# Optimization experiments

Measured on AMD Instinct MI355X. Metric: run time of the kernel, lower is better.

The kernel has to match this reference:

```python
import jax, jax.numpy as jnp
import numpy as np

SS = 25.0 / 255.0   # spatial_scale = 1 / (SEARCH_SIZE/25), SEARCH_SIZE = 255
OUT = 7             # ROIPOOL_OUTSIZE // 4, ROIPOOL_OUTSIZE = 28
SP = 4              # sample_per_part (mmdet DeformRoIPooling default)
TRANS_STD = 0.1


def _deform_roi_pool(x, rois, offset):
    # x: [B,C,H,W]; rois: [N,5] (batch_idx,x1,y1,x2,y2); offset: [N,2,OUT,OUT] (ch0=x, ch1=y)
    B, C, H, W = x.shape
    N = rois.shape[0]
    b = rois[:, 0].astype(jnp.int32)
    sw = jnp.round(rois[:, 1]) * SS - 0.5
    sh = jnp.round(rois[:, 2]) * SS - 0.5
    rw = jnp.maximum((jnp.round(rois[:, 3]) + 1.0) * SS - 0.5 - sw, 0.1)
    rh = jnp.maximum((jnp.round(rois[:, 4]) + 1.0) * SS - 0.5 - sh, 0.1)
    bw, bh = rw / OUT, rh / OUT
    p = jnp.arange(OUT, dtype=x.dtype)
    tx = offset[:, 0] * TRANS_STD  # [N,OUT,OUT] indexed [n,ph,pw]
    ty = offset[:, 1] * TRANS_STD
    wstart = p[None, None, :] * bw[:, None, None] + sw[:, None, None] + tx * rw[:, None, None]
    hstart = p[None, :, None] * bh[:, None, None] + sh[:, None, None] + ty * rh[:, None, None]
    s = jnp.arange(SP, dtype=x.dtype)
    # sample coords [N,OUT,OUT,SP(ih),SP(iw)]
    sx = wstart[..., None, None] + s[None, None, None, None, :] * (bw / SP)[:, None, None, None, None]
    sy = hstart[..., None, None] + s[None, None, None, :, None] * (bh / SP)[:, None, None, None, None]
    valid = (sx >= -0.5) & (sx <= W - 0.5) & (sy >= -0.5) & (sy <= H - 0.5)
    xc = jnp.clip(sx, 0.0, W - 1.0)
    yc = jnp.clip(sy, 0.0, H - 1.0)
    x0 = jnp.floor(xc)
    y0 = jnp.floor(yc)
    dx = xc - x0
    dy = yc - y0
    xi0 = x0.astype(jnp.int32)
    yi0 = y0.astype(jnp.int32)
    xi1 = jnp.ceil(xc).astype(jnp.int32)
    yi1 = jnp.ceil(yc).astype(jnp.int32)
    feat = jnp.transpose(x, (0, 2, 3, 1))  # [B,H,W,C]
    bb = b[:, None, None, None, None]

    def g(yi, xi):
        return feat[bb, yi, xi]  # [N,OUT,OUT,SP,SP,C]

    val = (((1 - dx) * (1 - dy))[..., None] * g(yi0, xi0)
           + (dx * (1 - dy))[..., None] * g(yi0, xi1)
           + ((1 - dx) * dy)[..., None] * g(yi1, xi0)
           + (dx * dy)[..., None] * g(yi1, xi1))
    val = jnp.where(valid[..., None], val, 0.0)
    cnt = valid.sum(axis=(3, 4)).astype(x.dtype)              # [N,OUT,OUT]
    pooled = val.sum(axis=(3, 4)) / jnp.maximum(cnt, 1.0)[..., None]
    return jnp.transpose(pooled, (0, 3, 1, 2))                # [N,C,OUT,OUT]


def _lin(h, w, b):
    return h @ w.T + b


def _forward(x, rois, off_w1, off_b1, off_w2, off_b2, off_w3, off_b3,
             fc1_w, fc1_b, fc2_w, fc2_b, box_w, box_b):
    N = rois.shape[0]
    zero_off = jnp.zeros((N, 2, OUT, OUT), x.dtype)
    # pass 1: no-trans pooling -> offset prediction
    p0 = _deform_roi_pool(x, rois, zero_off).reshape(N, -1)
    h = jax.nn.relu(_lin(p0, off_w1, off_b1))
    h = jax.nn.relu(_lin(h, off_w2, off_b2))
    off = _lin(h, off_w3, off_b3).reshape(N, 2, OUT, OUT)
    # pass 2: deformable pooling with predicted offsets
    p = _deform_roi_pool(x, rois, off).reshape(N, -1)
    h = jax.nn.relu(_lin(p, fc1_w, fc1_b))
    h = jax.nn.relu(_lin(h, fc2_w, fc2_b))
    return _lin(h, box_w, box_b)  # [N,4]


def setup_inputs():
    key = jax.random.key(0)
    ks = jax.random.split(key, 16)
    B, C, H, W, N = 8, 256, 25, 25, 256
    IN = C * OUT * OUT  # 12544
    DFC, FCC = 1024, 512
    x = jax.random.normal(ks[0], (B, C, H, W), jnp.float32)
    bidx = jax.random.randint(ks[1], (N,), 0, B).astype(jnp.float32)
    x1 = jax.random.uniform(ks[2], (N,), minval=0.0, maxval=180.0)
    y1 = jax.random.uniform(ks[3], (N,), minval=0.0, maxval=180.0)
    wd = jax.random.uniform(ks[4], (N,), minval=24.0, maxval=120.0)
    ht = jax.random.uniform(ks[5], (N,), minval=24.0, maxval=120.0)
    rois = jnp.stack([bidx, x1, y1, jnp.clip(x1 + wd, 0.0, 254.0),
                      jnp.clip(y1 + ht, 0.0, 254.0)], axis=1)

    def lin_p(k, o, i):
        return jax.random.normal(k, (o, i), jnp.float32) * (1.0 / np.sqrt(i))

    return dict(
        x=x, rois=rois,
        off_w1=lin_p(ks[6], DFC, IN), off_b1=jnp.zeros((DFC,), jnp.float32),
        off_w2=lin_p(ks[7], DFC, DFC), off_b2=jnp.zeros((DFC,), jnp.float32),
        off_w3=lin_p(ks[8], 2 * OUT * OUT, DFC) * 0.1,
        off_b3=jnp.zeros((2 * OUT * OUT,), jnp.float32),
        fc1_w=lin_p(ks[9], FCC, IN), fc1_b=jnp.zeros((FCC,), jnp.float32),
        fc2_w=lin_p(ks[10], FCC, FCC), fc2_b=jnp.zeros((FCC,), jnp.float32),
        box_w=lin_p(ks[11], 4, FCC) * 0.001, box_b=jnp.zeros((4,), jnp.float32),
    )


def reference(x, rois, off_w1, off_b1, off_w2, off_b2, off_w3, off_b3,
              fc1_w, fc1_b, fc2_w, fc2_b, box_w, box_b):
    return _forward(x, rois, off_w1, off_b1, off_w2, off_b2, off_w3, off_b3,
                    fc1_w, fc1_b, fc2_w, fc2_b, box_w, box_b)
```

## Files before the change

kernel.cpp:

```cpp
#include <hip/hip_runtime.h>
#include <hip/hip_bf16.h>


#define NROI 256
#define NB   8
#define INF  12544
#define DFC  1024
#define FCC  512

typedef __attribute__((ext_vector_type(8))) short short8;
typedef __attribute__((ext_vector_type(4))) float floatx4;

static __device__ __forceinline__ unsigned short f2bf(float f) {
    unsigned int u = __float_as_uint(f);
    unsigned int r = (u + 0x7fffu + ((u >> 16) & 1u)) >> 16;
    return (unsigned short)r;
}

static __device__ __forceinline__ void async_copy16(const void* g, void* l) {
    __builtin_amdgcn_global_load_lds(
        (const __attribute__((address_space(1))) unsigned int*)g,
        (__attribute__((address_space(3))) unsigned int*)l, 16, 0, 0);
}

__global__ __launch_bounds__(256) void transpose_kernel(
        const float* __restrict__ x, float* __restrict__ xT) {
    __shared__ float t[32][33];
    int b  = blockIdx.z;
    int cb = blockIdx.y * 32;
    int lb = blockIdx.x * 32;
    int tx = threadIdx.x & 31, ty = threadIdx.x >> 5;
#pragma unroll
    for (int r = 0; r < 4; ++r) {
        int c = cb + ty + r * 8, l = lb + tx;
        if (l < 625) t[ty + r * 8][tx] = x[(size_t)(b * 256 + c) * 625 + l];
    }
    __syncthreads();
#pragma unroll
    for (int r = 0; r < 4; ++r) {
        int l = lb + ty + r * 8, c = cb + tx;
        if (l < 625) xT[((size_t)b * 625 + l) * 256 + c] = t[tx][ty + r * 8];
    }
}

__global__ __launch_bounds__(256) void pool_kernel(
        const float* __restrict__ feat, const float* __restrict__ rois,
        const float* __restrict__ off, int has_off,
        unsigned short* __restrict__ P) {
    __shared__ float sGrid[49][16];
    __shared__ int   sBase[49];
    __shared__ unsigned short sOut[128 * 49];
    const float SSC = (float)(25.0 / 255.0);
    int q = blockIdx.x;
    int n = blockIdx.y;
    int tid = threadIdx.x;

    if (tid < 49) {
        int bin = tid;
        const float* r = rois + n * 5;
        int b = (int)r[0];
        float sw = rintf(r[1]) * SSC - 0.5f;
        float sh = rintf(r[2]) * SSC - 0.5f;
        float rw = fmaxf((rintf(r[3]) + 1.0f) * SSC - 0.5f - sw, 0.1f);
        float rh = fmaxf((rintf(r[4]) + 1.0f) * SSC - 0.5f - sh, 0.1f);
        float bw = rw / 7.0f, bh = rh / 7.0f;
        float bws = bw * 0.25f, bhs = bh * 0.25f;
        int ph = bin / 7, pw = bin - ph * 7;
        float tx = 0.f, ty = 0.f;
        if (has_off) {
            tx = off[n * 98 + bin] * 0.1f;
            ty = off[n * 98 + 49 + bin] * 0.1f;
        }
        float wstart = pw * bw + sw + tx * rw;
        float hstart = ph * bh + sh + ty * rh;
#pragma unroll
        for (int i = 0; i < 16; ++i) sGrid[bin][i] = 0.f;
        int gy0 = 0, gx0 = 0, cnt = 0;
#pragma unroll
        for (int s = 0; s < 16; ++s) {
            float fx = wstart + (s & 3) * bws;
            float fy = hstart + (s >> 2) * bhs;
            bool valid = (fx >= -0.5f) && (fx <= 24.5f) && (fy >= -0.5f) && (fy <= 24.5f);
            float xc = fminf(fmaxf(fx, 0.f), 24.f);
            float yc = fminf(fmaxf(fy, 0.f), 24.f);
            float x0f = floorf(xc), y0f = floorf(yc);
            float dx = xc - x0f, dy = yc - y0f;
            int x0 = (int)x0f, y0 = (int)y0f;
            int x1 = (int)ceilf(xc), y1 = (int)ceilf(yc);
            if (s == 0) { gy0 = y0; gx0 = x0; }
            float w00 = (1.f - dx) * (1.f - dy), w01 = dx * (1.f - dy);
            float w10 = (1.f - dx) * dy,         w11 = dx * dy;
            if (!valid) { w00 = w01 = w10 = w11 = 0.f; }
            cnt += valid ? 1 : 0;
            int ry0 = (y0 - gy0) * 4, ry1 = (y1 - gy0) * 4;
            sGrid[bin][ry0 + (x0 - gx0)] += w00;
            sGrid[bin][ry0 + (x1 - gx0)] += w01;
            sGrid[bin][ry1 + (x0 - gx0)] += w10;
            sGrid[bin][ry1 + (x1 - gx0)] += w11;
        }
        float inv = 1.0f / fmaxf((float)cnt, 1.0f);
#pragma unroll
        for (int i = 0; i < 16; ++i) sGrid[bin][i] *= inv;
        sBase[bin] = gy0 | (gx0 << 8) | (b << 16);
    }
    __syncthreads();

    int wv = tid >> 6, lane = tid & 63;
    int cbase = q * 128 + lane * 2;
    for (int bin = wv; bin < 49; bin += 4) {
        int base = sBase[bin];
        int gy0 = base & 255, gx0 = (base >> 8) & 255, b = base >> 16;
        const float4* wp = (const float4*)sGrid[bin];
        float4 w0 = wp[0], w1 = wp[1], w2 = wp[2], w3 = wp[3];
        float ww[16] = { w0.x, w0.y, w0.z, w0.w, w1.x, w1.y, w1.z, w1.w,
                         w2.x, w2.y, w2.z, w2.w, w3.x, w3.y, w3.z, w3.w };
        int rowOff[4], colOff[4];
#pragma unroll
        for (int r = 0; r < 4; ++r) {
            rowOff[r] = min(gy0 + r, 24) * 25;
            colOff[r] = min(gx0 + r, 24);
        }
        int b625 = b * 625;
        float ax = 0.f, ay = 0.f;
#pragma unroll
        for (int cell = 0; cell < 16; ++cell) {
            int pix = b625 + rowOff[cell >> 2] + colOff[cell & 3];
            float2 v = *(const float2*)(feat + (size_t)pix * 256 + cbase);
            ax += ww[cell] * v.x;
            ay += ww[cell] * v.y;
        }
        sOut[(lane * 2) * 49 + bin] = f2bf(ax);
        sOut[(lane * 2 + 1) * 49 + bin] = f2bf(ay);
    }
    __syncthreads();
    const uint2* so = (const uint2*)sOut;
    uint2* dp = (uint2*)(P + (size_t)n * INF + q * 128 * 49);
    for (int i = tid; i < 128 * 49 / 4; i += 256) dp[i] = so[i];
}

__global__ __launch_bounds__(256) void gemm_pipe(
        const unsigned short* __restrict__ A, const float* __restrict__ Bw,
        float* __restrict__ Cpart, int N, int K, int kSteps) {
    constexpr int BM = 256, BN = 32, D = 3;
    constexpr int FM = 4, FN = 2;
    __shared__ unsigned short As[D][BM * 32];
    __shared__ float          Bs[D][BN * 32];
    const int tid = threadIdx.x;
    const int lane = tid & 63;
    const int wave = tid >> 6;
    const int n0 = blockIdx.x * BN;
    const int k0 = blockIdx.z * kSteps * 32;
    const int quad = lane >> 4;
    const int l16 = lane & 15;

    floatx4 acc[FM][FN];
#pragma unroll
    for (int i = 0; i < FM; ++i)
#pragma unroll
        for (int j = 0; j < FN; ++j) acc[i][j] = (floatx4)0.f;

    const unsigned short* ag[4];
    int albase[4];
#pragma unroll
    for (int i = 0; i < 4; ++i) {
        int idx = tid + i * 256;
        int row = idx >> 2;
        int kg4 = (idx & 3) ^ ((row >> 1) & 3);
        ag[i] = A + (size_t)row * K + kg4 * 8;
        albase[i] = (i * 256 + wave * 64) * 16;
    }
    const int brow = tid >> 3;
    const int bkg = (tid & 7) ^ ((brow >> 1) & 7);
    const float* bg = Bw + (size_t)(n0 + brow) * K + bkg * 4;
    const int blbase = wave * 64 * 16;

    auto issue = [&](int slot, int kk) {
#pragma unroll
        for (int i = 0; i < 4; ++i)
            async_copy16(ag[i] + kk, (char*)&As[slot][0] + albase[i]);
        async_copy16(bg + kk, (char*)&Bs[slot][0] + blbase);
    };

#pragma unroll
    for (int p = 0; p < D - 1; ++p) {
        int pk = (p < kSteps) ? p : (kSteps - 1);
        issue(p, k0 + pk * 32);
    }

    int cur = 0;
    for (int ks = 0; ks < kSteps; ++ks) {
        asm volatile("s_waitcnt vmcnt(5)" ::: "memory");
        asm volatile("s_barrier" ::: "memory");
        int pfs = cur + D - 1; if (pfs >= D) pfs -= D;
        int pfk = ks + D - 1; if (pfk >= kSteps) pfk = kSteps - 1;
        issue(pfs, k0 + pfk * 32);
        short8 a[FM], bf[FN];
#pragma unroll
        for (int i = 0; i < FM; ++i) {
            int r = wave * 64 + i * 16 + l16;
            int sl = quad ^ ((r >> 1) & 3);
            a[i] = *(const short8*)(&As[cur][0] + r * 32 + sl * 8);
        }
#pragma unroll
        for (int j = 0; j < FN; ++j) {
            int r = j * 16 + l16;
            int sw8 = (r >> 1) & 7;
            int g0 = (quad * 2) ^ sw8;
            int g1 = (quad * 2 + 1) ^ sw8;
            float4 v0 = *(const float4*)(&Bs[cur][0] + r * 32 + g0 * 4);
            float4 v1 = *(const float4*)(&Bs[cur][0] + r * 32 + g1 * 4);
            bf[j][0] = (short)f2bf(v0.x); bf[j][1] = (short)f2bf(v0.y);
            bf[j][2] = (short)f2bf(v0.z); bf[j][3] = (short)f2bf(v0.w);
            bf[j][4] = (short)f2bf(v1.x); bf[j][5] = (short)f2bf(v1.y);
            bf[j][6] = (short)f2bf(v1.z); bf[j][7] = (short)f2bf(v1.w);
        }
#pragma unroll
        for (int i = 0; i < FM; ++i)
#pragma unroll
            for (int j = 0; j < FN; ++j)
                acc[i][j] = __builtin_amdgcn_mfma_f32_16x16x32_bf16(a[i], bf[j], acc[i][j], 0, 0, 0);
        cur = cur + 1; if (cur >= D) cur = 0;
    }
    float* Cp = Cpart + (size_t)blockIdx.z * BM * N;
#pragma unroll
    for (int i = 0; i < FM; ++i)
#pragma unroll
        for (int rr = 0; rr < 4; ++rr) {
            int row = wave * 64 + i * 16 + quad * 4 + rr;
            float* cr = Cp + (size_t)row * N + n0;
#pragma unroll
            for (int j = 0; j < FN; ++j)
                cr[j * 16 + l16] = acc[i][j][rr];
        }
}

__global__ __launch_bounds__(256) void reduce_bias(
        const float* __restrict__ part, int zc, int mn4,
        const float* __restrict__ bias, int nmask, int relu,
        unsigned short* __restrict__ obf, float* __restrict__ of) {
    int idx = blockIdx.x * 256 + threadIdx.x;
    if (idx >= mn4) return;
    int idx4 = idx * 4;
    const float* bp = bias + (idx4 & nmask);
    float4 acc = *(const float4*)bp;
    const float4* p = (const float4*)part + idx;
    for (int z = 0; z < zc; ++z) {
        float4 v = p[(size_t)z * mn4];
        acc.x += v.x; acc.y += v.y; acc.z += v.z; acc.w += v.w;
    }
    if (relu) {
        acc.x = fmaxf(acc.x, 0.f); acc.y = fmaxf(acc.y, 0.f);
        acc.z = fmaxf(acc.z, 0.f); acc.w = fmaxf(acc.w, 0.f);
    }
    if (obf) {
        ushort4 h;
        h.x = f2bf(acc.x); h.y = f2bf(acc.y); h.z = f2bf(acc.z); h.w = f2bf(acc.w);
        *(ushort4*)(obf + idx4) = h;
    }
    if (of) *(float4*)(of + idx4) = acc;
}

__global__ __launch_bounds__(256) void fc_small(
        const float* __restrict__ h2, const float* __restrict__ w3,
        const float* __restrict__ b3, float* __restrict__ out) {
    __shared__ float shl[2][1024];
    int n2 = blockIdx.x * 2;
    int tid = threadIdx.x;
    for (int i = tid; i < 2048; i += 256)
        shl[i >> 10][i & 1023] = fmaxf(h2[(size_t)n2 * 1024 + i], 0.f);
    __syncthreads();
    int h = tid >> 7, o = tid & 127;
    if (o < 98) {
        float acc = b3[o];
        const float* w = w3 + (size_t)o * 1024;
        const float* s = shl[h];
        for (int k = 0; k < 1024; k += 4) {
            float4 wv = *(const float4*)(w + k);
            acc += s[k] * wv.x + s[k + 1] * wv.y + s[k + 2] * wv.z + s[k + 3] * wv.w;
        }
        out[(n2 + h) * 98 + o] = acc;
    }
}

__global__ __launch_bounds__(64) void head_kernel(
        const float* __restrict__ h4, const float* __restrict__ bw,
        const float* __restrict__ bb, float* __restrict__ out) {
    int n = blockIdx.x, t = threadIdx.x;
    float a0 = 0, a1 = 0, a2 = 0, a3 = 0;
    for (int k = t; k < 512; k += 64) {
        float v = fmaxf(h4[(size_t)n * 512 + k], 0.f);
        a0 += v * bw[k]; a1 += v * bw[512 + k];
        a2 += v * bw[1024 + k]; a3 += v * bw[1536 + k];
    }
#pragma unroll
    for (int o = 32; o > 0; o >>= 1) {
        a0 += __shfl_down(a0, o); a1 += __shfl_down(a1, o);
        a2 += __shfl_down(a2, o); a3 += __shfl_down(a3, o);
    }
    if (t == 0) {
        out[n * 4 + 0] = a0 + bb[0]; out[n * 4 + 1] = a1 + bb[1];
        out[n * 4 + 2] = a2 + bb[2]; out[n * 4 + 3] = a3 + bb[3];
    }
}

extern "C" void kernel_launch(void* const* d_in, const int* in_sizes, int n_in,
                              void* d_out, int out_size, void* d_ws, size_t ws_size,
                              hipStream_t stream) {
    const float* x      = (const float*)d_in[0];
    const float* rois   = (const float*)d_in[1];
    const float* off_w1 = (const float*)d_in[2];
    const float* off_b1 = (const float*)d_in[3];
    const float* off_w2 = (const float*)d_in[4];
    const float* off_b2 = (const float*)d_in[5];
    const float* off_w3 = (const float*)d_in[6];
    const float* off_b3 = (const float*)d_in[7];
    const float* fc1_w  = (const float*)d_in[8];
    const float* fc1_b  = (const float*)d_in[9];
    const float* fc2_w  = (const float*)d_in[10];
    const float* fc2_b  = (const float*)d_in[11];
    const float* box_w  = (const float*)d_in[12];
    const float* box_b  = (const float*)d_in[13];
    float* out = (float*)d_out;

    char* ws = (char*)d_ws;
    size_t o = 0;
    auto carve = [&](size_t bytes) { char* p = ws + o; o += (bytes + 255) & ~(size_t)255; return p; };
    float*          xT   = (float*)carve((size_t)NB * 625 * 256 * 4);
    unsigned short* P    = (unsigned short*)carve((size_t)NROI * INF * 2);
    unsigned short* h1b  = (unsigned short*)carve((size_t)NROI * DFC * 2);
    float*          h2   = (float*)carve((size_t)NROI * DFC * 4);
    float*          offb = (float*)carve((size_t)NROI * 98 * 4);
    unsigned short* h3b  = (unsigned short*)carve((size_t)NROI * FCC * 2);
    float*          h4   = (float*)carve((size_t)NROI * FCC * 4);
    size_t fixed = o;
    const size_t SLAB = (size_t)NROI * DFC * 4;
    int zg1;
    if      (ws_size >= fixed + 28 * SLAB) zg1 = 28;
    else if (ws_size >= fixed + 14 * SLAB) zg1 = 14;
    else                                   zg1 = 7;
    float* part = (float*)carve((size_t)zg1 * SLAB);

    transpose_kernel<<<dim3(20, 8, 8), 256, 0, stream>>>(x, xT);
    pool_kernel<<<dim3(2, NROI), 256, 0, stream>>>(xT, rois, nullptr, 0, P);
    gemm_pipe<<<dim3(32, 1, zg1), 256, 0, stream>>>(P, off_w1, part, DFC, INF, 392 / zg1);
    reduce_bias<<<256, 256, 0, stream>>>(part, zg1, NROI * DFC / 4, off_b1, DFC - 1, 1, h1b, nullptr);
    gemm_pipe<<<dim3(32, 1, 8), 256, 0, stream>>>(h1b, off_w2, part, DFC, DFC, 4);
    reduce_bias<<<256, 256, 0, stream>>>(part, 8, NROI * DFC / 4, off_b2, DFC - 1, 0, nullptr, h2);
    fc_small<<<128, 256, 0, stream>>>(h2, off_w3, off_b3, offb);
    pool_kernel<<<dim3(2, NROI), 256, 0, stream>>>(xT, rois, offb, 1, P);
    gemm_pipe<<<dim3(16, 1, zg1), 256, 0, stream>>>(P, fc1_w, part, FCC, INF, 392 / zg1);
    reduce_bias<<<128, 256, 0, stream>>>(part, zg1, NROI * FCC / 4, fc1_b, FCC - 1, 1, h3b, nullptr);
    gemm_pipe<<<dim3(16, 1, 8), 256, 0, stream>>>(h3b, fc2_w, part, FCC, FCC, 2);
    reduce_bias<<<128, 256, 0, stream>>>(part, 8, NROI * FCC / 4, fc2_b, FCC - 1, 0, nullptr, h4);
    head_kernel<<<NROI, 64, 0, stream>>>(h4, box_w, box_b, out);
}
```

Baseline: 302.7 us.

## Fuse all stages into one persistent kernel with atomic grid barriers

```diff
diff --git a/kernel.cpp b/kernel.cpp
--- a/kernel.cpp
+++ b/kernel.cpp
@@ -23,36 +23,53 @@
         (__attribute__((address_space(3))) unsigned int*)l, 16, 0, 0);
 }
 
-__global__ __launch_bounds__(256) void transpose_kernel(
-        const float* __restrict__ x, float* __restrict__ xT) {
-    __shared__ float t[32][33];
-    int b  = blockIdx.z;
-    int cb = blockIdx.y * 32;
-    int lb = blockIdx.x * 32;
-    int tx = threadIdx.x & 31, ty = threadIdx.x >> 5;
-#pragma unroll
-    for (int r = 0; r < 4; ++r) {
-        int c = cb + ty + r * 8, l = lb + tx;
-        if (l < 625) t[ty + r * 8][tx] = x[(size_t)(b * 256 + c) * 625 + l];
-    }
-    __syncthreads();
-#pragma unroll
-    for (int r = 0; r < 4; ++r) {
-        int l = lb + ty + r * 8, c = cb + tx;
-        if (l < 625) xT[((size_t)b * 625 + l) * 256 + c] = t[tx][ty + r * 8];
-    }
-}
-
-__global__ __launch_bounds__(256) void pool_kernel(
+union SMem {
+    struct { float t[32][33]; } tr;
+    struct { float grid[49][16]; int base[49];
+             unsigned short out[128 * 49]; } pool;
+    struct { unsigned short As[3][256 * 32]; float Bs[3][32 * 32]; } gm;
+    struct { float h[1024]; } fc;
+};
+
+static __device__ __forceinline__ void gridbar(unsigned* ctr, int idx, unsigned nblk) {
+    __syncthreads();
+    if (threadIdx.x == 0) {
+        __hip_atomic_fetch_add(&ctr[idx], 1u, __ATOMIC_ACQ_REL, __HIP_MEMORY_SCOPE_AGENT);
+        while (__hip_atomic_load(&ctr[idx], __ATOMIC_ACQUIRE, __HIP_MEMORY_SCOPE_AGENT) < nblk)
+            __builtin_amdgcn_s_sleep(1);
+    }
+    __syncthreads();
+}
+
+static __device__ __forceinline__ void phase_transpose(
+        const float* __restrict__ x, float* __restrict__ xT, SMem& sm) {
+    int tid = threadIdx.x;
+    int tx = tid & 31, ty = tid >> 5;
+    for (int t = blockIdx.x; t < 1280; t += gridDim.x) {
+        int b = t / 160, rem = t - b * 160;
+        int cb = (rem / 20) * 32, lb = (rem % 20) * 32;
+#pragma unroll
+        for (int r = 0; r < 4; ++r) {
+            int c = cb + ty + r * 8, l = lb + tx;
+            if (l < 625) sm.tr.t[ty + r * 8][tx] = x[(size_t)(b * 256 + c) * 625 + l];
+        }
+        __syncthreads();
+#pragma unroll
+        for (int r = 0; r < 4; ++r) {
+            int l = lb + ty + r * 8, c = cb + tx;
+            if (l < 625) xT[((size_t)b * 625 + l) * 256 + c] = sm.tr.t[tx][ty + r * 8];
+        }
+        __syncthreads();
+    }
+}
+
+static __device__ __forceinline__ void phase_pool(
         const float* __restrict__ feat, const float* __restrict__ rois,
         const float* __restrict__ off, int has_off,
-        unsigned short* __restrict__ P) {
-    __shared__ float sGrid[49][16];
-    __shared__ int   sBase[49];
-    __shared__ unsigned short sOut[128 * 49];
+        unsigned short* __restrict__ P, SMem& sm) {
     const float SSC = (float)(25.0 / 255.0);
-    int q = blockIdx.x;
-    int n = blockIdx.y;
+    int q = blockIdx.x >> 8;
+    int n = blockIdx.x & 255;
     int tid = threadIdx.x;
 
     if (tid < 49) {
@@ -74,7 +91,7 @@
         float wstart = pw * bw + sw + tx * rw;
         float hstart = ph * bh + sh + ty * rh;
 #pragma unroll
-        for (int i = 0; i < 16; ++i) sGrid[bin][i] = 0.f;
+        for (int i = 0; i < 16; ++i) sm.pool.grid[bin][i] = 0.f;
         int gy0 = 0, gx0 = 0, cnt = 0;
 #pragma unroll
         for (int s = 0; s < 16; ++s) {
@@ -93,24 +110,24 @@
             if (!valid) { w00 = w01 = w10 = w11 = 0.f; }
             cnt += valid ? 1 : 0;
             int ry0 = (y0 - gy0) * 4, ry1 = (y1 - gy0) * 4;
-            sGrid[bin][ry0 + (x0 - gx0)] += w00;
-            sGrid[bin][ry0 + (x1 - gx0)] += w01;
-            sGrid[bin][ry1 + (x0 - gx0)] += w10;
-            sGrid[bin][ry1 + (x1 - gx0)] += w11;
+            sm.pool.grid[bin][ry0 + (x0 - gx0)] += w00;
+            sm.pool.grid[bin][ry0 + (x1 - gx0)] += w01;
+            sm.pool.grid[bin][ry1 + (x0 - gx0)] += w10;
+            sm.pool.grid[bin][ry1 + (x1 - gx0)] += w11;
         }
         float inv = 1.0f / fmaxf((float)cnt, 1.0f);
 #pragma unroll
-        for (int i = 0; i < 16; ++i) sGrid[bin][i] *= inv;
-        sBase[bin] = gy0 | (gx0 << 8) | (b << 16);
+        for (int i = 0; i < 16; ++i) sm.pool.grid[bin][i] *= inv;
+        sm.pool.base[bin] = gy0 | (gx0 << 8) | (b << 16);
     }
     __syncthreads();
 
     int wv = tid >> 6, lane = tid & 63;
     int cbase = q * 128 + lane * 2;
     for (int bin = wv; bin < 49; bin += 4) {
-        int base = sBase[bin];
+        int base = sm.pool.base[bin];
         int gy0 = base & 255, gx0 = (base >> 8) & 255, b = base >> 16;
-        const float4* wp = (const float4*)sGrid[bin];
+        const float4* wp = (const float4*)sm.pool.grid[bin];
         float4 w0 = wp[0], w1 = wp[1], w2 = wp[2], w3 = wp[3];
         float ww[16] = { w0.x, w0.y, w0.z, w0.w, w1.x, w1.y, w1.z, w1.w,
                          w2.x, w2.y, w2.z, w2.w, w3.x, w3.y, w3.z, w3.w };
@@ -129,35 +146,33 @@
             ax += ww[cell] * v.x;
             ay += ww[cell] * v.y;
         }
-        sOut[(lane * 2) * 49 + bin] = f2bf(ax);
-        sOut[(lane * 2 + 1) * 49 + bin] = f2bf(ay);
-    }
-    __syncthreads();
-    const uint2* so = (const uint2*)sOut;
+        sm.pool.out[(lane * 2) * 49 + bin] = f2bf(ax);
+        sm.pool.out[(lane * 2 + 1) * 49 + bin] = f2bf(ay);
+    }
+    __syncthreads();
+    const uint2* so = (const uint2*)sm.pool.out;
     uint2* dp = (uint2*)(P + (size_t)n * INF + q * 128 * 49);
     for (int i = tid; i < 128 * 49 / 4; i += 256) dp[i] = so[i];
 }
 
-__global__ __launch_bounds__(256) void gemm_pipe(
+static __device__ __forceinline__ void gemm_phase(
         const unsigned short* __restrict__ A, const float* __restrict__ Bw,
-        float* __restrict__ Cpart, int N, int K, int kSteps) {
-    constexpr int BM = 256, BN = 32, D = 3;
-    constexpr int FM = 4, FN = 2;
-    __shared__ unsigned short As[D][BM * 32];
-    __shared__ float          Bs[D][BN * 32];
+        float* __restrict__ Cpart, int N, int K, int nT, int zN, SMem& sm) {
+    const int blk = blockIdx.x;
+    if (blk >= nT * zN) return;
     const int tid = threadIdx.x;
-    const int lane = tid & 63;
-    const int wave = tid >> 6;
-    const int n0 = blockIdx.x * BN;
-    const int k0 = blockIdx.z * kSteps * 32;
-    const int quad = lane >> 4;
-    const int l16 = lane & 15;
-
-    floatx4 acc[FM][FN];
-#pragma unroll
-    for (int i = 0; i < FM; ++i)
-#pragma unroll
-        for (int j = 0; j < FN; ++j) acc[i][j] = (floatx4)0.f;
+    const int lane = tid & 63, wave = tid >> 6;
+    const int quad = lane >> 4, l16 = lane & 15;
+    const int nt = blk % nT, zi = blk / nT;
+    const int n0 = nt * 32;
+    const int kTot = K >> 5;
+    const int kPerZ = kTot / zN, rem = kTot % zN;
+    const int kStart = zi * kPerZ + (zi < rem ? zi : rem);
+    const int kCount = kPerZ + (zi < rem ? 1 : 0);
+
+    floatx4 acc[4][2];
+#pragma unroll
+    for (int i = 0; i < 4; ++i) { acc[i][0] = (floatx4)0.f; acc[i][1] = (floatx4)0.f; }
 
     const unsigned short* ag[4];
     int albase[4];
@@ -175,74 +190,69 @@
     const int blbase = wave * 64 * 16;
 
     auto issue = [&](int slot, int kk) {
+        int ke = kk * 32;
 #pragma unroll
         for (int i = 0; i < 4; ++i)
-            async_copy16(ag[i] + kk, (char*)&As[slot][0] + albase[i]);
-        async_copy16(bg + kk, (char*)&Bs[slot][0] + blbase);
+            async_copy16(ag[i] + ke, (char*)&sm.gm.As[slot][0] + albase[i]);
+        async_copy16(bg + ke, (char*)&sm.gm.Bs[slot][0] + blbase);
     };
 
-#pragma unroll
-    for (int p = 0; p < D - 1; ++p) {
-        int pk = (p < kSteps) ? p : (kSteps - 1);
-        issue(p, k0 + pk * 32);
-    }
+    issue(0, kStart);
+    issue(1, kStart + (kCount > 1 ? 1 : 0));
 
     int cur = 0;
-    for (int ks = 0; ks < kSteps; ++ks) {
+    for (int ks = 0; ks < kCount; ++ks) {
         asm volatile("s_waitcnt vmcnt(5)" ::: "memory");
         asm volatile("s_barrier" ::: "memory");
-        int pfs = cur + D - 1; if (pfs >= D) pfs -= D;
-        int pfk = ks + D - 1; if (pfk >= kSteps) pfk = kSteps - 1;
-        issue(pfs, k0 + pfk * 32);
-        short8 a[FM], bf[FN];
-#pragma unroll
-        for (int i = 0; i < FM; ++i) {
+        int pfs = cur + 2; if (pfs >= 3) pfs -= 3;
+        int pfk = ks + 2; if (pfk > kCount - 1) pfk = kCount - 1;
+        issue(pfs, kStart + pfk);
+        short8 a[4], bf[2];
+#pragma unroll
+        for (int i = 0; i < 4; ++i) {
             int r = wave * 64 + i * 16 + l16;
             int sl = quad ^ ((r >> 1) & 3);
-            a[i] = *(const short8*)(&As[cur][0] + r * 32 + sl * 8);
-        }
-#pragma unroll
-        for (int j = 0; j < FN; ++j) {
+            a[i] = *(const short8*)(&sm.gm.As[cur][0] + r * 32 + sl * 8);
+        }
+#pragma unroll
+        for (int j = 0; j < 2; ++j) {
             int r = j * 16 + l16;
             int sw8 = (r >> 1) & 7;
-            int g0 = (quad * 2) ^ sw8;
-            int g1 = (quad * 2 + 1) ^ sw8;
-            float4 v0 = *(const float4*)(&Bs[cur][0] + r * 32 + g0 * 4);
-            float4 v1 = *(const float4*)(&Bs[cur][0] + r * 32 + g1 * 4);
+            int g0 = (quad * 2) ^ sw8, g1 = (quad * 2 + 1) ^ sw8;
+            float4 v0 = *(const float4*)(&sm.gm.Bs[cur][0] + r * 32 + g0 * 4);
+            float4 v1 = *(const float4*)(&sm.gm.Bs[cur][0] + r * 32 + g1 * 4);
             bf[j][0] = (short)f2bf(v0.x); bf[j][1] = (short)f2bf(v0.y);
             bf[j][2] = (short)f2bf(v0.z); bf[j][3] = (short)f2bf(v0.w);
             bf[j][4] = (short)f2bf(v1.x); bf[j][5] = (short)f2bf(v1.y);
             bf[j][6] = (short)f2bf(v1.z); bf[j][7] = (short)f2bf(v1.w);
         }
 #pragma unroll
-        for (int i = 0; i < FM; ++i)
-#pragma unroll
-            for (int j = 0; j < FN; ++j)
+        for (int i = 0; i < 4; ++i)
+#pragma unroll
+            for (int j = 0; j < 2; ++j)
                 acc[i][j] = __builtin_amdgcn_mfma_f32_16x16x32_bf16(a[i], bf[j], acc[i][j], 0, 0, 0);
-        cur = cur + 1; if (cur >= D) cur = 0;
-    }
-    float* Cp = Cpart + (size_t)blockIdx.z * BM * N;
-#pragma unroll
-    for (int i = 0; i < FM; ++i)
+        cur = cur + 1; if (cur >= 3) cur = 0;
+    }
+    float* Cp = Cpart + (size_t)zi * 256 * N;
+#pragma unroll
+    for (int i = 0; i < 4; ++i)
 #pragma unroll
         for (int rr = 0; rr < 4; ++rr) {
             int row = wave * 64 + i * 16 + quad * 4 + rr;
             float* cr = Cp + (size_t)row * N + n0;
-#pragma unroll
-            for (int j = 0; j < FN; ++j)
-                cr[j * 16 + l16] = acc[i][j][rr];
-        }
-}
-
-__global__ __launch_bounds__(256) void reduce_bias(
+            cr[l16] = acc[i][0][rr];
+            cr[16 + l16] = acc[i][1][rr];
+        }
+}
+
+static __device__ __forceinline__ void phase_reduce(
         const float* __restrict__ part, int zc, int mn4,
         const float* __restrict__ bias, int nmask, int relu,
         unsigned short* __restrict__ obf, float* __restrict__ of) {
     int idx = blockIdx.x * 256 + threadIdx.x;
     if (idx >= mn4) return;
     int idx4 = idx * 4;
-    const float* bp = bias + (idx4 & nmask);
-    float4 acc = *(const float4*)bp;
+    float4 acc = *(const float4*)(bias + (idx4 & nmask));
     const float4* p = (const float4*)part + idx;
     for (int z = 0; z < zc; ++z) {
         float4 v = p[(size_t)z * mn4];
@@ -260,47 +270,70 @@
     if (of) *(float4*)(of + idx4) = acc;
 }
 
-__global__ __launch_bounds__(256) void fc_small(
+static __device__ __forceinline__ void phase_fc(
         const float* __restrict__ h2, const float* __restrict__ w3,
-        const float* __restrict__ b3, float* __restrict__ out) {
-    __shared__ float shl[2][1024];
-    int n2 = blockIdx.x * 2;
-    int tid = threadIdx.x;
-    for (int i = tid; i < 2048; i += 256)
-        shl[i >> 10][i & 1023] = fmaxf(h2[(size_t)n2 * 1024 + i], 0.f);
-    __syncthreads();
-    int h = tid >> 7, o = tid & 127;
-    if (o < 98) {
-        float acc = b3[o];
-        const float* w = w3 + (size_t)o * 1024;
-        const float* s = shl[h];
+        const float* __restrict__ b3, float* __restrict__ outp, SMem& sm) {
+    if (blockIdx.x >= 256) return;
+    int n = blockIdx.x, tid = threadIdx.x;
+    for (int i = tid; i < 1024; i += 256)
+        sm.fc.h[i] = fmaxf(h2[(size_t)n * 1024 + i], 0.f);
+    __syncthreads();
+    if (tid < 98) {
+        float acc = b3[tid];
+        const float* w = w3 + (size_t)tid * 1024;
         for (int k = 0; k < 1024; k += 4) {
             float4 wv = *(const float4*)(w + k);
-            acc += s[k] * wv.x + s[k + 1] * wv.y + s[k + 2] * wv.z + s[k + 3] * wv.w;
-        }
-        out[(n2 + h) * 98 + o] = acc;
-    }
-}
-
-__global__ __launch_bounds__(64) void head_kernel(
+            acc += sm.fc.h[k] * wv.x + sm.fc.h[k + 1] * wv.y +
+                   sm.fc.h[k + 2] * wv.z + sm.fc.h[k + 3] * wv.w;
+        }
+        outp[n * 98 + tid] = acc;
+    }
+}
+
+static __device__ __forceinline__ void phase_head(
         const float* __restrict__ h4, const float* __restrict__ bw,
         const float* __restrict__ bb, float* __restrict__ out) {
-    int n = blockIdx.x, t = threadIdx.x;
-    float a0 = 0, a1 = 0, a2 = 0, a3 = 0;
-    for (int k = t; k < 512; k += 64) {
-        float v = fmaxf(h4[(size_t)n * 512 + k], 0.f);
-        a0 += v * bw[k]; a1 += v * bw[512 + k];
-        a2 += v * bw[1024 + k]; a3 += v * bw[1536 + k];
-    }
-#pragma unroll
-    for (int o = 32; o > 0; o >>= 1) {
-        a0 += __shfl_down(a0, o); a1 += __shfl_down(a1, o);
-        a2 += __shfl_down(a2, o); a3 += __shfl_down(a3, o);
-    }
-    if (t == 0) {
-        out[n * 4 + 0] = a0 + bb[0]; out[n * 4 + 1] = a1 + bb[1];
-        out[n * 4 + 2] = a2 + bb[2]; out[n * 4 + 3] = a3 + bb[3];
-    }
+    if (blockIdx.x >= 256) return;
+    int n = blockIdx.x;
+    int wave = threadIdx.x >> 6, lane = threadIdx.x & 63;
+    const float* w = bw + wave * 512;
+    const float* h = h4 + (size_t)n * 512;
+    float a = 0.f;
+#pragma unroll
+    for (int i = 0; i < 8; ++i) {
+        int k = lane + i * 64;
+        a += fmaxf(h[k], 0.f) * w[k];
+    }
+#pragma unroll
+    for (int o = 32; o > 0; o >>= 1) a += __shfl_down(a, o);
+    if (lane == 0) out[n * 4 + wave] = a + bb[wave];
+}
+
+__global__ __launch_bounds__(256, 2) void mega_kernel(
+        const float* x, const float* rois,
+        const float* w1, const float* b1, const float* w2, const float* b2,
+        const float* w3, const float* b3, const float* fw1, const float* fb1,
+        const float* fw2, const float* fb2, const float* bxw, const float* bxb,
+        float* out, unsigned* ctr,
+        float* xT, unsigned short* P, unsigned short* h1b, float* h2,
+        float* offb, unsigned short* h3b, float* h4, float* part,
+        int z1, int z2, int z4, int z5) {
+    __shared__ SMem sm;
+    const unsigned nb = gridDim.x;
+
+    phase_transpose(x, xT, sm);                                gridbar(ctr, 0, nb);
+    phase_pool(xT, rois, nullptr, 0, P, sm);                   gridbar(ctr, 1, nb);
+    gemm_phase(P, w1, part, DFC, INF, 32, z1, sm);             gridbar(ctr, 2, nb);
+    phase_reduce(part, z1, NROI * DFC / 4, b1, DFC - 1, 1, h1b, nullptr); gridbar(ctr, 3, nb);
+    gemm_phase(h1b, w2, part, DFC, DFC, 32, z2, sm);           gridbar(ctr, 4, nb);
+    phase_reduce(part, z2, NROI * DFC / 4, b2, DFC - 1, 0, nullptr, h2);  gridbar(ctr, 5, nb);
+    phase_fc(h2, w3, b3, offb, sm);                            gridbar(ctr, 6, nb);
+    phase_pool(xT, rois, offb, 1, P, sm);                      gridbar(ctr, 7, nb);
+    gemm_phase(P, fw1, part, FCC, INF, 16, z4, sm);            gridbar(ctr, 8, nb);
+    phase_reduce(part, z4, NROI * FCC / 4, fb1, FCC - 1, 1, h3b, nullptr); gridbar(ctr, 9, nb);
+    gemm_phase(h3b, fw2, part, FCC, FCC, 16, z5, sm);          gridbar(ctr, 10, nb);
+    phase_reduce(part, z5, NROI * FCC / 4, fb2, FCC - 1, 0, nullptr, h4);  gridbar(ctr, 11, nb);
+    phase_head(h4, bxw, bxb, out);
 }
 
 extern "C" void kernel_launch(void* const* d_in, const int* in_sizes, int n_in,
@@ -325,6 +358,7 @@
     char* ws = (char*)d_ws;
     size_t o = 0;
     auto carve = [&](size_t bytes) { char* p = ws + o; o += (bytes + 255) & ~(size_t)255; return p; };
+    unsigned*       ctr  = (unsigned*)carve(256);
     float*          xT   = (float*)carve((size_t)NB * 625 * 256 * 4);
     unsigned short* P    = (unsigned short*)carve((size_t)NROI * INF * 2);
     unsigned short* h1b  = (unsigned short*)carve((size_t)NROI * DFC * 2);
@@ -334,23 +368,15 @@
     float*          h4   = (float*)carve((size_t)NROI * FCC * 4);
     size_t fixed = o;
     const size_t SLAB = (size_t)NROI * DFC * 4;
-    int zg1;
-    if      (ws_size >= fixed + 28 * SLAB) zg1 = 28;
-    else if (ws_size >= fixed + 14 * SLAB) zg1 = 14;
-    else                                   zg1 = 7;
-    float* part = (float*)carve((size_t)zg1 * SLAB);
-
-    transpose_kernel<<<dim3(20, 8, 8), 256, 0, stream>>>(x, xT);
-    pool_kernel<<<dim3(2, NROI), 256, 0, stream>>>(xT, rois, nullptr, 0, P);
-    gemm_pipe<<<dim3(32, 1, zg1), 256, 0, stream>>>(P, off_w1, part, DFC, INF, 392 / zg1);
-    reduce_bias<<<256, 256, 0, stream>>>(part, zg1, NROI * DFC / 4, off_b1, DFC - 1, 1, h1b, nullptr);
-    gemm_pipe<<<dim3(32, 1, 8), 256, 0, stream>>>(h1b, off_w2, part, DFC, DFC, 4);
-    reduce_bias<<<256, 256, 0, stream>>>(part, 8, NROI * DFC / 4, off_b2, DFC - 1, 0, nullptr, h2);
-    fc_small<<<128, 256, 0, stream>>>(h2, off_w3, off_b3, offb);
-    pool_kernel<<<dim3(2, NROI), 256, 0, stream>>>(xT, rois, offb, 1, P);
-    gemm_pipe<<<dim3(16, 1, zg1), 256, 0, stream>>>(P, fc1_w, part, FCC, INF, 392 / zg1);
-    reduce_bias<<<128, 256, 0, stream>>>(part, zg1, NROI * FCC / 4, fc1_b, FCC - 1, 1, h3b, nullptr);
-    gemm_pipe<<<dim3(16, 1, 8), 256, 0, stream>>>(h3b, fc2_w, part, FCC, FCC, 2);
-    reduce_bias<<<128, 256, 0, stream>>>(part, 8, NROI * FCC / 4, fc2_b, FCC - 1, 0, nullptr, h4);
-    head_kernel<<<NROI, 64, 0, stream>>>(h4, box_w, box_b, out);
-}
+    int z1, z2, z4, z5 = 16;
+    if      (ws_size >= fixed + 16 * SLAB) { z1 = 16; z2 = 16; z4 = 32; }
+    else if (ws_size >= fixed +  8 * SLAB) { z1 = 8;  z2 = 8;  z4 = 16; }
+    else                                   { z1 = 4;  z2 = 4;  z4 = 8; z5 = 8; }
+    float* part = (float*)carve((size_t)z1 * SLAB);
+
+    hipMemsetAsync(ctr, 0, 256, stream);
+    mega_kernel<<<512, 256, 0, stream>>>(
+        x, rois, off_w1, off_b1, off_w2, off_b2, off_w3, off_b3,
+        fc1_w, fc1_b, fc2_w, fc2_b, box_w, box_b,
+        out, ctr, xT, P, h1b, h2, offb, h3b, h4, part, z1, z2, z4, z5);
+}
```

New measurement: 1.056 ms. 3.49x slower.
